# Kernel tuning notes

Measured on AMD Instinct MI355X. Metric: run time of the kernel, lower is better.

Reference implementation:

```python
import jax, jax.numpy as jnp
import numpy as np

B, Tt, Ta, Tv = 2048, 128, 256, 256
D, E, R, H, L, NC = 64, 4, 8, 4, 4, 7
SCALING = 16.0 / 8.0  # alpha / r


def _ln(x, g, b, eps=1e-5):
    m = x.mean(-1, keepdims=True)
    v = ((x - m) ** 2).mean(-1, keepdims=True)
    return (x - m) / jnp.sqrt(v + eps) * g + b


def setup_inputs() -> dict:
    key = jax.random.key(0)
    ks = iter(jax.random.split(key, 64))
    def rn(shape, s=0.05):
        return jax.random.normal(next(ks), shape, jnp.float32) * s
    d = {}
    d['text'] = jax.random.normal(next(ks), (B, Tt, 300), jnp.float32)
    d['audio'] = jax.random.normal(next(ks), (B, Ta, 74), jnp.float32)
    d['video'] = jax.random.normal(next(ks), (B, Tv, 35), jnp.float32)
    # modality projections (Linear + LayerNorm)
    d['text_w'] = rn((300, D)); d['text_b'] = jnp.zeros(D); d['text_ln_g'] = jnp.ones(D); d['text_ln_b'] = jnp.zeros(D)
    d['audio_w'] = rn((74, D)); d['audio_b'] = jnp.zeros(D); d['audio_ln_g'] = jnp.ones(D); d['audio_ln_b'] = jnp.zeros(D)
    d['video_w'] = rn((35, D)); d['video_b'] = jnp.zeros(D); d['video_ln_g'] = jnp.ones(D); d['video_ln_b'] = jnp.zeros(D)
    d['latent'] = rn((1, L, D), 0.02)
    # cross-attention in/out projections
    d['wq'] = rn((D, D)); d['bq'] = jnp.zeros(D)
    d['wk'] = rn((D, D)); d['bk'] = jnp.zeros(D)
    d['wv'] = rn((D, D)); d['bv'] = jnp.zeros(D)
    d['wo'] = rn((D, D)); d['bo'] = jnp.zeros(D)
    d['n1_g'] = jnp.ones(D); d['n1_b'] = jnp.zeros(D)
    d['ffn_w1'] = rn((D, 4 * D)); d['ffn_b1'] = jnp.zeros(4 * D)
    d['ffn_w2'] = rn((4 * D, D)); d['ffn_b2'] = jnp.zeros(D)
    d['n2_g'] = jnp.ones(D); d['n2_b'] = jnp.zeros(D)
    # router
    d['r_w1'] = rn((D, D)); d['r_b1'] = jnp.zeros(D)
    d['r_ln_g'] = jnp.ones(D); d['r_ln_b'] = jnp.zeros(D)
    d['r_w2'] = rn((D, E)); d['r_b2'] = jnp.zeros(E)
    d['p1_w'] = rn((D, D // 2)); d['p1_b'] = jnp.zeros(D // 2)
    d['p2_w'] = rn((D, D // 2)); d['p2_b'] = jnp.zeros(D // 2)
    # LoRA experts, stacked: down [E,D,R], up [E,R,D]
    d['lora_down'] = rn((E, D, R), 0.1)
    d['lora_up'] = rn((E, R, D), 0.1)
    # classifier
    d['c_ln_g'] = jnp.ones(D); d['c_ln_b'] = jnp.zeros(D)
    d['c_w1'] = rn((D, D), 0.02); d['c_b1'] = jnp.zeros(D)
    d['c_w2'] = rn((D, NC), 0.02); d['c_b2'] = jnp.zeros(NC)
    return d


def reference(text, audio, video,
              text_w, text_b, text_ln_g, text_ln_b,
              audio_w, audio_b, audio_ln_g, audio_ln_b,
              video_w, video_b, video_ln_g, video_ln_b,
              latent, wq, bq, wk, bk, wv, bv, wo, bo,
              n1_g, n1_b, ffn_w1, ffn_b1, ffn_w2, ffn_b2, n2_g, n2_b,
              r_w1, r_b1, r_ln_g, r_ln_b, r_w2, r_b2,
              p1_w, p1_b, p2_w, p2_b,
              lora_down, lora_up,
              c_ln_g, c_ln_b, c_w1, c_b1, c_w2, c_b2):
    b = text.shape[0]
    def proj(x, w, bb, g, gb):  # Linear + LN + ReLU (dropout = eval identity)
        return jax.nn.relu(_ln(x @ w + bb, g, gb))
    # mean-pool each modality over time, project to d_model -> [b,3,D]
    zt = proj(text.mean(1), text_w, text_b, text_ln_g, text_ln_b)
    za = proj(audio.mean(1), audio_w, audio_b, audio_ln_g, audio_ln_b)
    zv = proj(video.mean(1), video_w, video_b, video_ln_g, video_ln_b)
    inputs = jnp.stack([zt, za, zv], axis=1)  # [b,3,D]
    lat = jnp.broadcast_to(latent, (b, L, D))
    # cross-attention: latent queries attend over 3 modality tokens
    hd = D // H
    q = (lat @ wq + bq).reshape(b, L, H, hd)
    k = (inputs @ wk + bk).reshape(b, -1, H, hd)
    v = (inputs @ wv + bv).reshape(b, -1, H, hd)
    scores = jnp.einsum('blhd,bshd->bhls', q, k) / jnp.sqrt(jnp.float32(hd))
    attn = jax.nn.softmax(scores, axis=-1)
    attn_out = jnp.einsum('bhls,bshd->blhd', attn, v).reshape(b, L, D) @ wo + bo
    lat = _ln(lat + attn_out, n1_g, n1_b)
    ffn = jax.nn.gelu(lat @ ffn_w1 + ffn_b1, approximate=False) @ ffn_w2 + ffn_b2
    lat = _ln(lat + ffn, n2_g, n2_b)
    f = lat.mean(1)  # [b,D] perceiver features
    # router
    r_logits = jax.nn.relu(_ln(f @ r_w1 + r_b1, r_ln_g, r_ln_b)) @ r_w2 + r_b2
    weights = jax.nn.softmax(r_logits, axis=-1)  # [b,E]
    view1 = f @ p1_w + p1_b
    view2 = f @ p2_w + p2_b
    # all LoRA experts as one batched grouped GEMM
    down = jnp.einsum('bd,edr->ber', f, lora_down)
    up = jnp.einsum('ber,erd->bed', down, lora_up) * SCALING
    expert_out = f[:, None, :] + up  # [b,E,D]
    fused = jnp.einsum('bed,be->bd', expert_out, weights)
    # classifier
    h = jax.nn.relu(_ln(fused, c_ln_g, c_ln_b) @ c_w1 + c_b1)
    logits = h @ c_w2 + c_b2
    return (logits, weights, fused, f, view1, view2)
```

## Files before the change

### kernel.cpp

```cpp
#include <hip/hip_runtime.h>
#include <math.h>
#include <string.h>

#define B_   2048
#define TT   128
#define TA   256
#define TV   256
#define CT   300
#define CA   74
#define CV   35
#define D    64
#define E_   4
#define R_   8
#define H_   4
#define L_   4
#define NC   7
#define POOLW 416

struct Params {
  const float *text, *audio, *video;
  const float *text_w, *text_b, *text_ln_g, *text_ln_b;
  const float *audio_w, *audio_b, *audio_ln_g, *audio_ln_b;
  const float *video_w, *video_b, *video_ln_g, *video_ln_b;
  const float *latent;
  const float *wq, *bq, *wk, *bk, *wv, *bv, *wo, *bo;
  const float *n1_g, *n1_b, *ffn_w1, *ffn_b1, *ffn_w2, *ffn_b2, *n2_g, *n2_b;
  const float *r_w1, *r_b1, *r_ln_g, *r_ln_b, *r_w2, *r_b2;
  const float *p1_w, *p1_b, *p2_w, *p2_b;
  const float *lora_down, *lora_up;
  const float *c_ln_g, *c_ln_b, *c_w1, *c_b1, *c_w2, *c_b2;
  float *out;
  const float *pool;
  const float *qbuf;
};

__device__ __forceinline__ float wsum(float v) {
#pragma unroll
  for (int m = 32; m >= 1; m >>= 1) v += __shfl_xor(v, m, 64);
  return v;
}
__device__ __forceinline__ float hsum16(float v) {
#pragma unroll
  for (int m = 8; m >= 1; m >>= 1) v += __shfl_xor(v, m, 64);
  return v;
}
#define WB() __builtin_amdgcn_wave_barrier()

__global__ __launch_bounds__(256) void pool_kernel(
    const float* __restrict__ text, const float* __restrict__ audio,
    const float* __restrict__ video, const float* __restrict__ latent,
    const float* __restrict__ wq, const float* __restrict__ bq,
    float* __restrict__ pool, float* __restrict__ qbuf) {
  const int b = blockIdx.x;
  const int m = blockIdx.y;
  const int tid = threadIdx.x;
  __shared__ __align__(16) float sbuf[912];

  if (m == 0) {
    const float* x = text + (size_t)b * (TT * CT);
    const int c4 = tid % 75, g = tid / 75;
    if (g < 3) {
      float4 acc = make_float4(0.f, 0.f, 0.f, 0.f);
      for (int t = g; t < TT; t += 3) {
        float4 v = *reinterpret_cast<const float4*>(x + t * CT + 4 * c4);
        acc.x += v.x; acc.y += v.y; acc.z += v.z; acc.w += v.w;
      }
      reinterpret_cast<float4*>(sbuf)[g * 75 + c4] = acc;
    }
    __syncthreads();
    if (tid < 75) {
      float4 a = reinterpret_cast<float4*>(sbuf)[tid];
      float4 bb = reinterpret_cast<float4*>(sbuf)[75 + tid];
      float4 c = reinterpret_cast<float4*>(sbuf)[150 + tid];
      float4 r;
      r.x = (a.x + bb.x + c.x) * (1.f / TT);
      r.y = (a.y + bb.y + c.y) * (1.f / TT);
      r.z = (a.z + bb.z + c.z) * (1.f / TT);
      r.w = (a.w + bb.w + c.w) * (1.f / TT);
      *reinterpret_cast<float4*>(pool + (size_t)b * POOLW + 4 * tid) = r;
    }
    if (b == 0) {
      const int l = tid >> 6, j = tid & 63;
      float acc = bq[j];
      for (int i = 0; i < D; ++i) acc += latent[l * D + i] * wq[i * D + j];
      qbuf[l * D + j] = acc;
    }
  } else if (m == 1) {
    const float* x = audio + (size_t)b * (TA * CA);
    const int c2 = tid % 37, g = tid / 37;
    if (g < 6) {
      float2 acc = make_float2(0.f, 0.f);
      for (int t = g; t < TA; t += 6) {
        float2 v = *reinterpret_cast<const float2*>(x + t * CA + 2 * c2);
        acc.x += v.x; acc.y += v.y;
      }
      reinterpret_cast<float2*>(sbuf)[g * 37 + c2] = acc;
    }
    __syncthreads();
    if (tid < 37) {
      float2 r = make_float2(0.f, 0.f);
#pragma unroll
      for (int g2 = 0; g2 < 6; ++g2) {
        float2 v = reinterpret_cast<float2*>(sbuf)[g2 * 37 + tid];
        r.x += v.x; r.y += v.y;
      }
      r.x *= (1.f / TA); r.y *= (1.f / TA);
      *reinterpret_cast<float2*>(pool + (size_t)b * POOLW + CT + 2 * tid) = r;
    }
  } else {
    const float* x = video + (size_t)b * (TV * CV);
    const int c = tid % 35, g = tid / 35;
    if (g < 7) {
      float acc = 0.f;
      for (int t = g; t < TV; t += 7) acc += x[t * CV + c];
      sbuf[g * 35 + c] = acc;
    }
    __syncthreads();
    if (tid < 35) {
      float r = 0.f;
#pragma unroll
      for (int g2 = 0; g2 < 7; ++g2) r += sbuf[g2 * 35 + tid];
      pool[(size_t)b * POOLW + CT + CA + tid] = r * (1.f / TV);
    }
  }
}

__global__ __launch_bounds__(256) void head_kernel(Params p) {
  const int tid = threadIdx.x;
  const int lane = tid & 63;
  const int w = tid >> 6;
  const int b = blockIdx.x * 4 + w;

  __shared__ float s_q[L_ * D];
  __shared__ float s_pool[4][POOLW];
  __shared__ float s_z[4][3 * D];
  __shared__ float s_k[4][3 * D];
  __shared__ float s_ao[4][L_ * D];
  __shared__ float s_lat1[4][L_ * D];
  __shared__ float s_h1[4][L_ * 256];
  __shared__ float s_f[4][D];
  __shared__ float s_down[4][E_ * R_];
  __shared__ float s_cl[4][D];

  s_q[tid] = p.qbuf[tid];
  for (int i = lane; i < CT + CA + CV; i += 64)
    s_pool[w][i] = p.pool[(size_t)b * POOLW + i];
  __syncthreads();

  {
    float acc = p.text_b[lane];
    for (int i = 0; i < CT; ++i) acc += s_pool[w][i] * p.text_w[i * D + lane];
    float mu = wsum(acc) * (1.f / D);
    float d = acc - mu;
    float var = wsum(d * d) * (1.f / D);
    s_z[w][0 * D + lane] =
        fmaxf(d * rsqrtf(var + 1e-5f) * p.text_ln_g[lane] + p.text_ln_b[lane], 0.f);

    acc = p.audio_b[lane];
    for (int i = 0; i < CA; ++i) acc += s_pool[w][CT + i] * p.audio_w[i * D + lane];
    mu = wsum(acc) * (1.f / D); d = acc - mu; var = wsum(d * d) * (1.f / D);
    s_z[w][1 * D + lane] =
        fmaxf(d * rsqrtf(var + 1e-5f) * p.audio_ln_g[lane] + p.audio_ln_b[lane], 0.f);

    acc = p.video_b[lane];
    for (int i = 0; i < CV; ++i) acc += s_pool[w][CT + CA + i] * p.video_w[i * D + lane];
    mu = wsum(acc) * (1.f / D); d = acc - mu; var = wsum(d * d) * (1.f / D);
    s_z[w][2 * D + lane] =
        fmaxf(d * rsqrtf(var + 1e-5f) * p.video_ln_g[lane] + p.video_ln_b[lane], 0.f);
  }
  WB();

  float vreg[3];
#pragma unroll
  for (int s = 0; s < 3; ++s) {
    float ak = p.bk[lane], av = p.bv[lane];
    for (int i = 0; i < D; ++i) {
      float z = s_z[w][s * D + i];
      ak += z * p.wk[i * D + lane];
      av += z * p.wv[i * D + lane];
    }
    s_k[w][s * D + lane] = ak;
    vreg[s] = av;
  }
  WB();

  float aw[L_][3];
#pragma unroll
  for (int l = 0; l < L_; ++l) {
    float sc0 = hsum16(s_q[l * D + lane] * s_k[w][0 * D + lane]) * 0.25f;
    float sc1 = hsum16(s_q[l * D + lane] * s_k[w][1 * D + lane]) * 0.25f;
    float sc2 = hsum16(s_q[l * D + lane] * s_k[w][2 * D + lane]) * 0.25f;
    float mx = fmaxf(sc0, fmaxf(sc1, sc2));
    float e0 = expf(sc0 - mx), e1 = expf(sc1 - mx), e2 = expf(sc2 - mx);
    float inv = 1.f / (e0 + e1 + e2);
    aw[l][0] = e0 * inv; aw[l][1] = e1 * inv; aw[l][2] = e2 * inv;
  }

#pragma unroll
  for (int l = 0; l < L_; ++l)
    s_ao[w][l * D + lane] = aw[l][0] * vreg[0] + aw[l][1] * vreg[1] + aw[l][2] * vreg[2];
  WB();

#pragma unroll
  for (int l = 0; l < L_; ++l) {
    float acc = p.bo[lane];
    for (int i = 0; i < D; ++i) acc += s_ao[w][l * D + i] * p.wo[i * D + lane];
    float x = p.latent[l * D + lane] + acc;
    float mu = wsum(x) * (1.f / D);
    float d = x - mu;
    float var = wsum(d * d) * (1.f / D);
    s_lat1[w][l * D + lane] = d * rsqrtf(var + 1e-5f) * p.n1_g[lane] + p.n1_b[lane];
  }
  WB();

  {
    float hacc[L_][4];
#pragma unroll
    for (int k = 0; k < 4; ++k) {
      float bb = p.ffn_b1[k * 64 + lane];
#pragma unroll
      for (int l = 0; l < L_; ++l) hacc[l][k] = bb;
    }
    for (int i = 0; i < D; ++i) {
      float x0 = s_lat1[w][0 * D + i], x1 = s_lat1[w][1 * D + i];
      float x2 = s_lat1[w][2 * D + i], x3 = s_lat1[w][3 * D + i];
#pragma unroll
      for (int k = 0; k < 4; ++k) {
        float wv = p.ffn_w1[i * 256 + k * 64 + lane];
        hacc[0][k] += x0 * wv; hacc[1][k] += x1 * wv;
        hacc[2][k] += x2 * wv; hacc[3][k] += x3 * wv;
      }
    }
#pragma unroll
    for (int l = 0; l < L_; ++l)
#pragma unroll
      for (int k = 0; k < 4; ++k) {
        float x = hacc[l][k];
        s_h1[w][l * 256 + k * 64 + lane] = 0.5f * x * (1.f + erff(x * 0.70710678118654752f));
      }
  }
  WB();

  float fl;
  {
    float fsum = 0.f;
#pragma unroll
    for (int l = 0; l < L_; ++l) {
      float acc = p.ffn_b2[lane];
      for (int m2 = 0; m2 < 256; ++m2) acc += s_h1[w][l * 256 + m2] * p.ffn_w2[m2 * D + lane];
      float x = s_lat1[w][l * D + lane] + acc;
      float mu = wsum(x) * (1.f / D);
      float d = x - mu;
      float var = wsum(d * d) * (1.f / D);
      fsum += d * rsqrtf(var + 1e-5f) * p.n2_g[lane] + p.n2_b[lane];
    }
    fl = 0.25f * fsum;
    s_f[w][lane] = fl;
    p.out[(size_t)B_ * 75 + (size_t)b * D + lane] = fl;
  }
  WB();

  float w0, w1, w2, w3;
  {
    float acc = p.r_b1[lane];
    for (int i = 0; i < D; ++i) acc += s_f[w][i] * p.r_w1[i * D + lane];
    float mu = wsum(acc) * (1.f / D);
    float d = acc - mu;
    float var = wsum(d * d) * (1.f / D);
    float rr = fmaxf(d * rsqrtf(var + 1e-5f) * p.r_ln_g[lane] + p.r_ln_b[lane], 0.f);
    float l0 = wsum(rr * p.r_w2[lane * E_ + 0]) + p.r_b2[0];
    float l1 = wsum(rr * p.r_w2[lane * E_ + 1]) + p.r_b2[1];
    float l2 = wsum(rr * p.r_w2[lane * E_ + 2]) + p.r_b2[2];
    float l3 = wsum(rr * p.r_w2[lane * E_ + 3]) + p.r_b2[3];
    float mx = fmaxf(fmaxf(l0, l1), fmaxf(l2, l3));
    float e0 = expf(l0 - mx), e1 = expf(l1 - mx), e2 = expf(l2 - mx), e3 = expf(l3 - mx);
    float inv = 1.f / (e0 + e1 + e2 + e3);
    w0 = e0 * inv; w1 = e1 * inv; w2 = e2 * inv; w3 = e3 * inv;
    float wsel = (lane == 0) ? w0 : (lane == 1) ? w1 : (lane == 2) ? w2 : w3;
    if (lane < E_) p.out[(size_t)B_ * 7 + (size_t)b * E_ + lane] = wsel;
  }

  {
    const float* PW = (lane < 32) ? p.p1_w : p.p2_w;
    const float* PB = (lane < 32) ? p.p1_b : p.p2_b;
    const int col = lane & 31;
    float acc = PB[col];
    for (int i = 0; i < D; ++i) acc += s_f[w][i] * PW[i * 32 + col];
    const size_t base = (lane < 32) ? (size_t)B_ * 139 : (size_t)B_ * 171;
    p.out[base + (size_t)b * 32 + col] = acc;
  }

  if (lane < E_ * R_) {
    const int e = lane >> 3, r = lane & 7;
    float acc = 0.f;
    for (int dd = 0; dd < D; ++dd) acc += s_f[w][dd] * p.lora_down[e * D * R_ + dd * R_ + r];
    s_down[w][lane] = acc;
  }
  WB();

  float fused;
  {
    const float we4[4] = {w0, w1, w2, w3};
    float acc = 0.f;
#pragma unroll
    for (int e = 0; e < E_; ++e) {
      float up = 0.f;
#pragma unroll
      for (int r = 0; r < R_; ++r)
        up += s_down[w][e * R_ + r] * p.lora_up[e * R_ * D + r * D + lane];
      acc += we4[e] * (fl + 2.0f * up);
    }
    fused = acc;
    p.out[(size_t)B_ * 11 + (size_t)b * D + lane] = fused;
  }

  {
    float mu = wsum(fused) * (1.f / D);
    float d = fused - mu;
    float var = wsum(d * d) * (1.f / D);
    s_cl[w][lane] = d * rsqrtf(var + 1e-5f) * p.c_ln_g[lane] + p.c_ln_b[lane];
  }
  WB();
  {
    float acc = p.c_b1[lane];
    for (int i = 0; i < D; ++i) acc += s_cl[w][i] * p.c_w1[i * D + lane];
    float h = fmaxf(acc, 0.f);
#pragma unroll
    for (int nc = 0; nc < NC; ++nc) {
      float lg = wsum(h * p.c_w2[lane * NC + nc]) + p.c_b2[nc];
      if (lane == nc) p.out[(size_t)b * NC + nc] = lg;
    }
  }
}

extern "C" void kernel_launch(void* const* d_in, const int* in_sizes, int n_in,
                              void* d_out, int out_size, void* d_ws, size_t ws_size,
                              hipStream_t stream) {
  (void)in_sizes; (void)n_in; (void)out_size; (void)ws_size;
  Params p;
  memcpy(&p, d_in, 50 * sizeof(void*));
  p.out = (float*)d_out;
  float* pool = (float*)d_ws;
  float* qbuf = pool + (size_t)B_ * POOLW;
  p.pool = pool;
  p.qbuf = qbuf;
  pool_kernel<<<dim3(B_, 3), dim3(256), 0, stream>>>(p.text, p.audio, p.video,
                                                     p.latent, p.wq, p.bq, pool, qbuf);
  head_kernel<<<dim3(B_ / 4), dim3(256), 0, stream>>>(p);
}
```

Measured before the change: 714.9 us.

## Fuse pooling and head kernels into one kernel with shared-memory pooled features

Merges the temporal-pooling kernel and the per-sample head kernel into a single launch in which each 256-thread block pools four samples and keeps the pooled vectors in shared memory instead of writing them to a workspace. Each block also recomputes the latent query projection locally rather than reading it from a global buffer. The FFN hidden buffer is shrunk to one row per wave, computed and consumed per latent, which cuts LDS use. The cost is only 512 blocks doing the bandwidth-heavy pooling, compared with 6144 before, so streaming the inputs may get less memory-level parallelism.

Result: faster. 698.9 us (-2.2%).

```diff
diff --git a/kernel.cpp b/kernel.cpp
--- a/kernel.cpp
+++ b/kernel.cpp
@@ -30,8 +30,6 @@
   const float *lora_down, *lora_up;
   const float *c_ln_g, *c_ln_b, *c_w1, *c_b1, *c_w2, *c_b2;
   float *out;
-  const float *pool;
-  const float *qbuf;
 };
 
 __device__ __forceinline__ float wsum(float v) {
@@ -46,105 +44,115 @@
 }
 #define WB() __builtin_amdgcn_wave_barrier()
 
-__global__ __launch_bounds__(256) void pool_kernel(
-    const float* __restrict__ text, const float* __restrict__ audio,
-    const float* __restrict__ video, const float* __restrict__ latent,
-    const float* __restrict__ wq, const float* __restrict__ bq,
-    float* __restrict__ pool, float* __restrict__ qbuf) {
-  const int b = blockIdx.x;
-  const int m = blockIdx.y;
+__global__ __launch_bounds__(256) void fused_kernel(Params p) {
   const int tid = threadIdx.x;
-  __shared__ __align__(16) float sbuf[912];
-
-  if (m == 0) {
-    const float* x = text + (size_t)b * (TT * CT);
+  const int lane = tid & 63;
+  const int w = tid >> 6;
+  const int b0 = blockIdx.x * 4;
+  const int b = b0 + w;
+
+  __shared__ __align__(16) float4 sbufT[3][4][75];
+  __shared__ __align__(8)  float2 sbufA[6][4][37];
+  __shared__ float sbufV[7][4][35];
+  __shared__ __align__(16) float s_pool[4][POOLW];
+  __shared__ float s_q[L_ * D];
+  __shared__ float s_z[4][3 * D];
+  __shared__ float s_k[4][3 * D];
+  __shared__ float s_ao[4][L_ * D];
+  __shared__ float s_lat1[4][L_ * D];
+  __shared__ float s_h1w[4][256];
+  __shared__ float s_f[4][D];
+  __shared__ float s_down[4][E_ * R_];
+  __shared__ float s_cl[4][D];
+
+  {
     const int c4 = tid % 75, g = tid / 75;
     if (g < 3) {
-      float4 acc = make_float4(0.f, 0.f, 0.f, 0.f);
+      float4 acc[4];
+#pragma unroll
+      for (int s = 0; s < 4; ++s) acc[s] = make_float4(0.f, 0.f, 0.f, 0.f);
       for (int t = g; t < TT; t += 3) {
-        float4 v = *reinterpret_cast<const float4*>(x + t * CT + 4 * c4);
-        acc.x += v.x; acc.y += v.y; acc.z += v.z; acc.w += v.w;
-      }
-      reinterpret_cast<float4*>(sbuf)[g * 75 + c4] = acc;
-    }
-    __syncthreads();
-    if (tid < 75) {
-      float4 a = reinterpret_cast<float4*>(sbuf)[tid];
-      float4 bb = reinterpret_cast<float4*>(sbuf)[75 + tid];
-      float4 c = reinterpret_cast<float4*>(sbuf)[150 + tid];
+#pragma unroll
+        for (int s = 0; s < 4; ++s) {
+          float4 v = *reinterpret_cast<const float4*>(
+              p.text + (size_t)(b0 + s) * (TT * CT) + t * CT + 4 * c4);
+          acc[s].x += v.x; acc[s].y += v.y; acc[s].z += v.z; acc[s].w += v.w;
+        }
+      }
+#pragma unroll
+      for (int s = 0; s < 4; ++s) sbufT[g][s][c4] = acc[s];
+    }
+  }
+  {
+    const int c2 = tid % 37, g = tid / 37;
+    if (g < 6) {
+      float2 acc[4];
+#pragma unroll
+      for (int s = 0; s < 4; ++s) acc[s] = make_float2(0.f, 0.f);
+      for (int t = g; t < TA; t += 6) {
+#pragma unroll
+        for (int s = 0; s < 4; ++s) {
+          float2 v = *reinterpret_cast<const float2*>(
+              p.audio + (size_t)(b0 + s) * (TA * CA) + t * CA + 2 * c2);
+          acc[s].x += v.x; acc[s].y += v.y;
+        }
+      }
+#pragma unroll
+      for (int s = 0; s < 4; ++s) sbufA[g][s][c2] = acc[s];
+    }
+  }
+  {
+    const int c = tid % 35, g = tid / 35;
+    if (g < 7) {
+      float acc[4] = {0.f, 0.f, 0.f, 0.f};
+      for (int t = g; t < TV; t += 7) {
+#pragma unroll
+        for (int s = 0; s < 4; ++s)
+          acc[s] += p.video[(size_t)(b0 + s) * (TV * CV) + t * CV + c];
+      }
+#pragma unroll
+      for (int s = 0; s < 4; ++s) sbufV[g][s][c] = acc[s];
+    }
+  }
+  {
+    const int l = tid >> 6, j = tid & 63;
+    float acc = p.bq[j];
+    for (int i = 0; i < D; ++i) acc += p.latent[l * D + i] * p.wq[i * D + j];
+    s_q[tid] = acc;
+  }
+  __syncthreads();
+
+  if (tid < 75) {
+#pragma unroll
+    for (int s = 0; s < 4; ++s) {
+      float4 a = sbufT[0][s][tid], bb = sbufT[1][s][tid], c = sbufT[2][s][tid];
       float4 r;
       r.x = (a.x + bb.x + c.x) * (1.f / TT);
       r.y = (a.y + bb.y + c.y) * (1.f / TT);
       r.z = (a.z + bb.z + c.z) * (1.f / TT);
       r.w = (a.w + bb.w + c.w) * (1.f / TT);
-      *reinterpret_cast<float4*>(pool + (size_t)b * POOLW + 4 * tid) = r;
-    }
-    if (b == 0) {
-      const int l = tid >> 6, j = tid & 63;
-      float acc = bq[j];
-      for (int i = 0; i < D; ++i) acc += latent[l * D + i] * wq[i * D + j];
-      qbuf[l * D + j] = acc;
-    }
-  } else if (m == 1) {
-    const float* x = audio + (size_t)b * (TA * CA);
-    const int c2 = tid % 37, g = tid / 37;
-    if (g < 6) {
-      float2 acc = make_float2(0.f, 0.f);
-      for (int t = g; t < TA; t += 6) {
-        float2 v = *reinterpret_cast<const float2*>(x + t * CA + 2 * c2);
-        acc.x += v.x; acc.y += v.y;
-      }
-      reinterpret_cast<float2*>(sbuf)[g * 37 + c2] = acc;
-    }
-    __syncthreads();
-    if (tid < 37) {
+      *reinterpret_cast<float4*>(&s_pool[s][4 * tid]) = r;
+    }
+  } else if (tid < 112) {
+    const int c2 = tid - 75;
+#pragma unroll
+    for (int s = 0; s < 4; ++s) {
       float2 r = make_float2(0.f, 0.f);
 #pragma unroll
-      for (int g2 = 0; g2 < 6; ++g2) {
-        float2 v = reinterpret_cast<float2*>(sbuf)[g2 * 37 + tid];
-        r.x += v.x; r.y += v.y;
-      }
+      for (int g = 0; g < 6; ++g) { float2 v = sbufA[g][s][c2]; r.x += v.x; r.y += v.y; }
       r.x *= (1.f / TA); r.y *= (1.f / TA);
-      *reinterpret_cast<float2*>(pool + (size_t)b * POOLW + CT + 2 * tid) = r;
-    }
-  } else {
-    const float* x = video + (size_t)b * (TV * CV);
-    const int c = tid % 35, g = tid / 35;
-    if (g < 7) {
-      float acc = 0.f;
-      for (int t = g; t < TV; t += 7) acc += x[t * CV + c];
-      sbuf[g * 35 + c] = acc;
-    }
-    __syncthreads();
-    if (tid < 35) {
+      *reinterpret_cast<float2*>(&s_pool[s][CT + 2 * c2]) = r;
+    }
+  } else if (tid < 147) {
+    const int c = tid - 112;
+#pragma unroll
+    for (int s = 0; s < 4; ++s) {
       float r = 0.f;
 #pragma unroll
-      for (int g2 = 0; g2 < 7; ++g2) r += sbuf[g2 * 35 + tid];
-      pool[(size_t)b * POOLW + CT + CA + tid] = r * (1.f / TV);
-    }
-  }
-}
-
-__global__ __launch_bounds__(256) void head_kernel(Params p) {
-  const int tid = threadIdx.x;
-  const int lane = tid & 63;
-  const int w = tid >> 6;
-  const int b = blockIdx.x * 4 + w;
-
-  __shared__ float s_q[L_ * D];
-  __shared__ float s_pool[4][POOLW];
-  __shared__ float s_z[4][3 * D];
-  __shared__ float s_k[4][3 * D];
-  __shared__ float s_ao[4][L_ * D];
-  __shared__ float s_lat1[4][L_ * D];
-  __shared__ float s_h1[4][L_ * 256];
-  __shared__ float s_f[4][D];
-  __shared__ float s_down[4][E_ * R_];
-  __shared__ float s_cl[4][D];
-
-  s_q[tid] = p.qbuf[tid];
-  for (int i = lane; i < CT + CA + CV; i += 64)
-    s_pool[w][i] = p.pool[(size_t)b * POOLW + i];
+      for (int g = 0; g < 7; ++g) r += sbufV[g][s][c];
+      s_pool[s][CT + CA + c] = r * (1.f / TV);
+    }
+  }
   __syncthreads();
 
   {
@@ -213,8 +221,8 @@
   }
   WB();
 
-  {
-    float hacc[L_][4];
+  float hacc[L_][4];
+  {
 #pragma unroll
     for (int k = 0; k < 4; ++k) {
       float bb = p.ffn_b1[k * 64 + lane];
@@ -231,28 +239,27 @@
         hacc[2][k] += x2 * wv; hacc[3][k] += x3 * wv;
       }
     }
-#pragma unroll
-    for (int l = 0; l < L_; ++l)
+  }
+
+  float fl;
+  {
+    float fsum = 0.f;
+#pragma unroll
+    for (int l = 0; l < L_; ++l) {
 #pragma unroll
       for (int k = 0; k < 4; ++k) {
         float x = hacc[l][k];
-        s_h1[w][l * 256 + k * 64 + lane] = 0.5f * x * (1.f + erff(x * 0.70710678118654752f));
-      }
-  }
-  WB();
-
-  float fl;
-  {
-    float fsum = 0.f;
-#pragma unroll
-    for (int l = 0; l < L_; ++l) {
+        s_h1w[w][k * 64 + lane] = 0.5f * x * (1.f + erff(x * 0.70710678118654752f));
+      }
+      WB();
       float acc = p.ffn_b2[lane];
-      for (int m2 = 0; m2 < 256; ++m2) acc += s_h1[w][l * 256 + m2] * p.ffn_w2[m2 * D + lane];
+      for (int m2 = 0; m2 < 256; ++m2) acc += s_h1w[w][m2] * p.ffn_w2[m2 * D + lane];
       float x = s_lat1[w][l * D + lane] + acc;
       float mu = wsum(x) * (1.f / D);
       float d = x - mu;
       float var = wsum(d * d) * (1.f / D);
       fsum += d * rsqrtf(var + 1e-5f) * p.n2_g[lane] + p.n2_b[lane];
+      WB();
     }
     fl = 0.25f * fsum;
     s_f[w][lane] = fl;
@@ -336,15 +343,9 @@
 extern "C" void kernel_launch(void* const* d_in, const int* in_sizes, int n_in,
                               void* d_out, int out_size, void* d_ws, size_t ws_size,
                               hipStream_t stream) {
-  (void)in_sizes; (void)n_in; (void)out_size; (void)ws_size;
+  (void)in_sizes; (void)n_in; (void)out_size; (void)d_ws; (void)ws_size;
   Params p;
   memcpy(&p, d_in, 50 * sizeof(void*));
   p.out = (float*)d_out;
-  float* pool = (float*)d_ws;
-  float* qbuf = pool + (size_t)B_ * POOLW;
-  p.pool = pool;
-  p.qbuf = qbuf;
-  pool_kernel<<<dim3(B_, 3), dim3(256), 0, stream>>>(p.text, p.audio, p.video,
-                                                     p.latent, p.wq, p.bq, pool, qbuf);
-  head_kernel<<<dim3(B_ / 4), dim3(256), 0, stream>>>(p);
+  fused_kernel<<<dim3(B_ / 4), dim3(256), 0, stream>>>(p);
 }
```
